# Kernel tuning notes

Hardware: AMD Instinct MI355X
Metric: run time of the kernel (lower is better)

Reference implementation:

```python
import jax, jax.numpy as jnp
import numpy as np

EPS = 1e-7
INF = 1e8
NUM_CLASSES = 80
SOFT_CENTER_RADIUS = 3.0
TOPK = 13
IOU_WEIGHT = 3.0
ALPHA = 1.0
BETA = 6.0
IMG = 640.0


def pairwise_iou(b1, b2):
    # b1: (B,N,4), b2: (B,M,4) in xyxy -> (B,N,M) IoU (mmdet BboxOverlaps2D, eps=1e-6)
    a1 = (b1[..., 2] - b1[..., 0]) * (b1[..., 3] - b1[..., 1])
    a2 = (b2[..., 2] - b2[..., 0]) * (b2[..., 3] - b2[..., 1])
    lt = jnp.maximum(b1[:, :, None, :2], b2[:, None, :, :2])
    rb = jnp.minimum(b1[:, :, None, 2:], b2[:, None, :, 2:])
    wh = jnp.clip(rb - lt, 0.0)
    inter = wh[..., 0] * wh[..., 1]
    union = a1[:, :, None] + a2[:, None, :] - inter
    return inter / jnp.maximum(union, 1e-6)


def _forward(pred_bboxes, pred_scores, priors, gt_labels, gt_bboxes, pad_bbox_flag):
    B, P, _ = pred_bboxes.shape
    G = gt_bboxes.shape[1]
    dt = pred_bboxes.dtype
    labels = gt_labels[..., 0]            # (B,G) int
    pad = pad_bbox_flag[..., 0]           # (B,G) float
    prior_xy = priors[:, :2]              # (P,2)
    strides = priors[:, 2]                # (P,)

    # ---- inside-gt test (find_inside_points, box_dim=4): (B,P,G) bool
    lt_ = prior_xy[None, :, None, :] - gt_bboxes[:, None, :, :2]
    rb_ = gt_bboxes[:, None, :, 2:] - prior_xy[None, :, None, :]
    is_in_gts = jnp.minimum(lt_.min(-1), rb_.min(-1)) > 0        # (B,P,G)
    is_in_gts_f = is_in_gts.astype(dt) * pad[:, None, :]         # masked by pad flag
    valid_mask = is_in_gts_f.sum(-1) > 0                          # (B,P)

    # ---- get_pos_mask (TaskAligned metric top-k) -> fg_mask_pre_prior
    overlaps = pairwise_iou(gt_bboxes, pred_bboxes)               # (B,G,P)
    scores_sig = jax.nn.sigmoid(pred_scores)                      # (B,P,C)
    scores_g = jnp.take_along_axis(scores_sig.transpose(0, 2, 1), labels[:, :, None], axis=1)  # (B,G,P)
    align = (scores_g ** ALPHA) * (overlaps ** BETA)              # (B,G,P)
    in_gts_gp = is_in_gts.transpose(0, 2, 1).astype(dt)           # (B,G,P)
    metrics = align * in_gts_gp
    _, topk_idxs = jax.lax.top_k(metrics, TOPK)                   # (B,G,TOPK)
    bb = jnp.arange(B)[:, None, None]
    gg = jnp.arange(G)[None, :, None]
    cnt = jnp.zeros((B, G, P), dt).at[bb, gg, topk_idxs].add(1.0)
    cnt = cnt * pad[:, :, None]
    is_in_topk = jnp.where(cnt > 1, 0.0, cnt)
    pos_mask = is_in_topk * in_gts_gp * pad[:, :, None]           # (B,G,P)
    # select_highest_overlaps: resolve priors matched to >1 gt via max IoU
    fg_pre = pos_mask.sum(1)                                      # (B,P)
    max_gt = overlaps.argmax(1)                                   # (B,P)
    is_max = (jnp.arange(G)[None, None, :] == max_gt[:, :, None]).astype(dt)  # (B,P,G)
    pos_mask = jnp.where((fg_pre > 1)[:, None, :], is_max.transpose(0, 2, 1), pos_mask)
    fg_mask_pre_prior = pos_mask.sum(1) > 0                       # (B,P) bool

    # ---- soft center prior
    gt_center = (gt_bboxes[..., :2] + gt_bboxes[..., 2:]) / 2.0   # (B,G,2)
    dist = jnp.sqrt(((prior_xy[None, :, None, :] - gt_center[:, None, :, :]) ** 2).sum(-1)) \
           / strides[None, :, None]                               # (B,P,G)
    dist = dist * valid_mask[..., None]
    soft_center_prior = jnp.power(10.0, dist - SOFT_CENTER_RADIUS)

    # ---- IoU cost
    pairwise_ious = pairwise_iou(pred_bboxes, gt_bboxes)          # (B,P,G)
    iou_cost = -jnp.log(pairwise_ious + EPS) * IOU_WEIGHT

    # ---- soft classification cost (QFL-style)
    logits = jnp.take_along_axis(pred_scores.transpose(0, 2, 1), labels[:, :, None], axis=1)
    logits = logits.transpose(0, 2, 1)                            # (B,P,G)
    scale = pairwise_ious - jax.nn.sigmoid(logits)
    bce = jnp.logaddexp(0.0, logits) - logits * pairwise_ious     # BCEWithLogits(logits, ious)
    cls_cost = bce * scale ** 2

    cost = cls_cost + iou_cost + soft_center_prior
    cost = jnp.where(valid_mask[..., None], cost, INF)            # (B,P,G)

    # ---- dynamic-k matching
    topk_ious, _ = jax.lax.top_k(pairwise_ious.transpose(0, 2, 1), TOPK)  # (B,G,TOPK)
    dynamic_ks = jnp.maximum(topk_ious.sum(-1).astype(jnp.int32), 1)      # (B,G)
    num_gts = pad.sum(-1).astype(jnp.int32)                                # (B,)
    sorted_idx = jnp.argsort(cost, axis=1)                                 # (B,P,G)
    ranks = jnp.arange(P)[None, :, None]
    gt_valid = jnp.arange(G)[None, :] < num_gts[:, None]                   # (B,G)
    sel = (ranks < dynamic_ks[:, None, :]) & gt_valid[:, None, :]          # (B,P,G), in sorted order
    bb2 = jnp.arange(B)[:, None, None]
    gg2 = jnp.arange(G)[None, None, :]
    matching = jnp.zeros((B, P, G), dt).at[bb2, sorted_idx, gg2].set(sel.astype(dt))
    multi = matching.sum(-1) > 1                                           # (B,P)
    argmin = cost.argmin(-1)                                               # (B,P)
    onehot_min = (jnp.arange(G)[None, None, :] == argmin[:, :, None]).astype(dt)
    matching = jnp.where(multi[..., None], onehot_min, matching)
    fg = matching.sum(-1) > 0                                              # (B,P)
    matched_ious = (matching * pairwise_ious).sum(-1)                      # (B,P)
    matched_gt_inds = matching.argmax(-1)                                  # (B,P)

    # ---- dense outputs (torch scatters into full-size tensors; same values here)
    assigned_labels = jnp.where(fg, jnp.take_along_axis(labels, matched_gt_inds, axis=1), NUM_CLASSES)
    assigned_labels_weights = jnp.ones((B, P), dt)
    assigned_bboxes = jnp.where(fg[..., None],
                                jnp.take_along_axis(gt_bboxes, matched_gt_inds[..., None].repeat(4, -1), axis=1),
                                0.0)
    assign_metrics = jnp.where(fg, matched_ious, 0.0)
    return assigned_labels, assigned_labels_weights, assigned_bboxes, assign_metrics, fg_mask_pre_prior


def setup_inputs() -> dict:
    key = jax.random.key(0)
    ks = jax.random.split(key, 6)
    B, G, C = 16, 100, 80
    # priors: anchor-free grid for 640x640, strides (8,16,32) -> P = 8400
    grids = []
    for s in (8, 16, 32):
        n = 640 // s
        xs = (np.arange(n, dtype=np.float32) + 0.5) * s
        yy, xx = np.meshgrid(xs, xs, indexing='ij')
        g = np.stack([xx.ravel(), yy.ravel(),
                      np.full(n * n, s, np.float32), np.full(n * n, s, np.float32)], -1)
        grids.append(g)
    priors = jnp.asarray(np.concatenate(grids, 0), jnp.float32)  # (8400, 4)
    P = priors.shape[0]

    def rand_boxes(k, shape):
        kc, kw = jax.random.split(k)
        cxy = jax.random.uniform(kc, shape + (2,), minval=0.0, maxval=IMG)
        wh = jax.random.uniform(kw, shape + (2,), minval=8.0, maxval=256.0)
        lt = jnp.clip(cxy - wh / 2, 0.0, IMG)
        rb = jnp.clip(cxy + wh / 2, 0.0, IMG)
        return jnp.concatenate([lt, rb], -1)

    pred_bboxes = rand_boxes(ks[0], (B, P))
    pred_scores = jax.random.normal(ks[1], (B, P, C), jnp.float32) * 2.0 - 2.0
    gt_bboxes = rand_boxes(ks[2], (B, G))
    gt_labels = jax.random.randint(ks[3], (B, G, 1), 0, C)
    n_valid = jax.random.randint(ks[4], (B,), 1, G + 1)
    pad_bbox_flag = (jnp.arange(G)[None, :] < n_valid[:, None]).astype(jnp.float32)[..., None]
    return {"pred_bboxes": pred_bboxes, "pred_scores": pred_scores, "priors": priors,
            "gt_labels": gt_labels, "gt_bboxes": gt_bboxes, "pad_bbox_flag": pad_bbox_flag}


def reference(pred_bboxes, pred_scores, priors, gt_labels, gt_bboxes, pad_bbox_flag):
    return _forward(pred_bboxes, pred_scores, priors, gt_labels, gt_bboxes, pad_bbox_flag)
```

## Files before the change

### kernel.cpp

```cpp
#include <hip/hip_runtime.h>
#include <cstdint>
#include <climits>
#include <cstddef>

#define TK 13
#define MAXG 128
#define CAP 192
#define NW 4
#define MCAP 24576
#define MAXCH 160

__device__ __forceinline__ float iou_fn(const float4 pb, const float4 gb){
  float pa = (pb.z - pb.x) * (pb.w - pb.y);
  float ga = (gb.z - gb.x) * (gb.w - gb.y);
  float ltx = fmaxf(pb.x, gb.x), lty = fmaxf(pb.y, gb.y);
  float rbx = fminf(pb.z, gb.z), rby = fminf(pb.w, gb.w);
  float w = fmaxf(rbx - ltx, 0.0f), h = fmaxf(rby - lty, 0.0f);
  float inter = w * h;
  float uni = pa + ga - inter;
  return inter / fmaxf(uni, 1e-6f);
}

__device__ __forceinline__ float sigmoid_f(float x){ return 1.0f / (1.0f + expf(-x)); }

__device__ __forceinline__ float cost_full(float iou, float s, float dist){
  float sig = sigmoid_f(s);
  float iouc = -logf(iou + 1e-7f) * 3.0f;
  float scale = iou - sig;
  float bce = fmaxf(s, 0.0f) + log1pf(expf(-fabsf(s))) - s * iou;
  float cls = bce * scale * scale;
  float soft = powf(10.0f, dist - 3.0f);
  return cls + iouc + soft;
}

__device__ __forceinline__ void bfly_max_u64(unsigned long long &v, int &l){
  #pragma unroll
  for (int off = 32; off >= 1; off >>= 1){
    unsigned long long ov = __shfl_xor(v, off);
    int ol = __shfl_xor(l, off);
    if (ov > v){ v = ov; l = ol; }
  }
}

__device__ __forceinline__ unsigned long long squeeze13(unsigned long long* buf, int& cnt, int lane){
  unsigned long long e0 = (lane < cnt) ? buf[lane] : 0ull;
  unsigned long long e1 = (lane + 64 < cnt) ? buf[lane + 64] : 0ull;
  unsigned long long e2 = (lane + 128 < cnt) ? buf[lane + 128] : 0ull;
  if (e0 < e2){ unsigned long long t = e0; e0 = e2; e2 = t; }
  if (e0 < e1){ unsigned long long t = e0; e0 = e1; e1 = t; }
  if (e1 < e2){ unsigned long long t = e1; e1 = e2; e2 = t; }
  unsigned long long T = 0;
  for (int r = 0; r < TK; ++r){
    unsigned long long m = e0; int l = lane;
    bfly_max_u64(m, l);
    if (lane == 0) buf[r] = m;
    T = m;
    if (lane == l){ e0 = e1; e1 = e2; e2 = 0ull; }
  }
  cnt = TK;
  return T;
}

__global__ __launch_bounds__(256) void k_valid(
    const float4* __restrict__ priors, const float4* __restrict__ pred_bboxes,
    const float4* __restrict__ gtb, const float* __restrict__ pad,
    unsigned long long* __restrict__ vmask, unsigned int* __restrict__ acc,
    unsigned int* __restrict__ mcnt,
    float4* __restrict__ predAB, float4* __restrict__ prAB, float* __restrict__ strC,
    int P, int G, int nCh)
{
  int b = blockIdx.y;
  int p = blockIdx.x * 256 + threadIdx.x;
  if (b == 0 && p == 0) *mcnt = 0u;
  __shared__ float4 sg[MAXG];
  __shared__ float sp[MAXG];
  for (int i = threadIdx.x; i < G; i += 256){ sg[i] = gtb[b*G + i]; sp[i] = pad[b*G + i]; }
  __syncthreads();
  int lane = threadIdx.x & 63;
  int ch = p >> 6;
  bool inb = p < P;
  float4 pr = inb ? priors[p] : make_float4(0,0,0,0);
  float4 pb = inb ? pred_bboxes[(size_t)b*P + p] : make_float4(0,0,0,0);
  bool v = false;
  if (inb){
    #pragma unroll 4
    for (int g = 0; g < G; ++g){
      float4 gb = sg[g];
      bool ig = (pr.x > gb.x) && (pr.y > gb.y) && (gb.z > pr.x) && (gb.w > pr.y);
      v = v || (ig && sp[g] > 0.5f);
    }
    acc[(size_t)b * P + p] = 0u;
  }
  unsigned long long m = __ballot(v);
  if (lane == 0 && ch < nCh) vmask[(size_t)b * nCh + ch] = m;
  float inf = __builtin_inff();
  float x1 = inb ? pb.x : inf,  y1 = inb ? pb.y : inf;
  float x2 = inb ? pb.z : -inf, y2 = inb ? pb.w : -inf;
  float px1 = inb ? pr.x : inf,  py1 = inb ? pr.y : inf;
  float px2 = inb ? pr.x : -inf, py2 = inb ? pr.y : -inf;
  #pragma unroll
  for (int off = 32; off >= 1; off >>= 1){
    x1 = fminf(x1, __shfl_xor(x1, off));  y1 = fminf(y1, __shfl_xor(y1, off));
    x2 = fmaxf(x2, __shfl_xor(x2, off));  y2 = fmaxf(y2, __shfl_xor(y2, off));
    px1 = fminf(px1, __shfl_xor(px1, off)); py1 = fminf(py1, __shfl_xor(py1, off));
    px2 = fmaxf(px2, __shfl_xor(px2, off)); py2 = fmaxf(py2, __shfl_xor(py2, off));
  }
  if (lane == 0 && ch < nCh){
    predAB[(size_t)b * nCh + ch] = make_float4(x1, y1, x2, y2);
    if (b == 0){ prAB[ch] = make_float4(px1, py1, px2, py2); strC[ch] = pr.z; }
  }
}

__global__ __launch_bounds__(256) void k_scan(
    const float4* __restrict__ pred_bboxes, const float* __restrict__ pred_scores,
    const float4* __restrict__ priors, const int* __restrict__ gt_labels,
    const float4* __restrict__ gtbb, const float* __restrict__ pad,
    const unsigned long long* __restrict__ vmask,
    const float4* __restrict__ predAB, const float4* __restrict__ prAB,
    const float* __restrict__ strC,
    unsigned int* __restrict__ acc, unsigned int* __restrict__ mcnt,
    unsigned int* __restrict__ mlist,
    int P, int G, int C, int nCh)
{
  int bg = blockIdx.x;
  if (pad[bg] <= 0.5f) return;
  int b = bg / G;
  int g = bg - b * G;
  int tid = threadIdx.x;
  int lane = tid & 63;
  int wv = tid >> 6;
  float4 gb = gtbb[bg];
  int lbl = gt_labels[bg];
  float gcx = (gb.x + gb.z) * 0.5f, gcy = (gb.y + gb.w) * 0.5f;
  size_t bP = (size_t)b * P;
  const unsigned long long* vmb = vmask + (size_t)b * nCh;
  const float4* pAB = predAB + (size_t)b * nCh;
  const unsigned B1E8 = __float_as_uint(1e8f);

  __shared__ unsigned long long bufM[NW*CAP], bufC[NW*CAP], bufI[NW*CAP];
  __shared__ uint2 sgeo[MAXCH];
  __shared__ unsigned long long svm[MAXCH];
  __shared__ unsigned int shwC, shwM, shwI;
  if (tid == 0){ shwC = 0xFFFFFFFFu; shwM = 0u; shwI = 0u; }
  for (int ch = tid; ch < nCh; ch += 256){
    float4 pA = pAB[ch];
    float4 rA = prAB[ch];
    float strc = strC[ch];
    bool geoI = !(pA.x < gb.z && pA.z > gb.x && pA.y < gb.w && pA.w > gb.y);
    bool geoM = !(rA.z > gb.x && rA.x < gb.z && rA.w > gb.y && rA.y < gb.w);
    float dxr = fmaxf(0.0f, fmaxf(rA.x - gcx, gcx - rA.z));
    float dyr = fmaxf(0.0f, fmaxf(rA.y - gcy, gcy - rA.w));
    float drr = sqrtf(dxr*dxr + dyr*dyr) / strc;
    sgeo[ch] = make_uint2((geoI ? 1u : 0u) | (geoM ? 2u : 0u), __float_as_uint(drr));
    svm[ch] = vmb[ch];
  }
  __syncthreads();
  unsigned long long* bM = bufM + wv*CAP;
  unsigned long long* bC = bufC + wv*CAP;
  unsigned long long* bI = bufI + wv*CAP;

  int cntM = 0, cntC = 0, cntI = 0;
  int zM = 0, zC = 0;
  unsigned long long Tm = 0ull, Tc = 0ull;
  unsigned long long Ti = 0x00000000FFFFFFFFull;
  unsigned cbits = 0xFFFFFFFFu, mBbits = 0u, iBb = 0u;
  float thr = 1e30f, mB = 0.0f;
  unsigned long long laneLT = (1ull << lane) - 1ull;

  for (int c = wv; c < nCh; c += NW){
    { unsigned sC = shwC; if (sC < cbits){ cbits = sC;
        thr = 3.0f + log10f(__uint_as_float(cbits) * 1.00002f + 1e-6f); } }
    { unsigned sM = shwM; if (sM > mBbits){ mBbits = sM; mB = __uint_as_float(sM); } }
    { unsigned sI = shwI; if (sI > iBb) iBb = sI; }
    uint2 ge = sgeo[c];
    bool geoI = (ge.x & 1u) != 0u;
    bool geoM = (ge.x & 2u) != 0u;
    float drr = __uint_as_float(ge.y);
    bool poolM = (zM >= TK) || (mBbits > 0u);
    bool poolC = (zC >= TK) || (cbits < B1E8);
    bool skipMt = geoM && poolM;
    bool skipCt = (drr > thr) && poolC;
    if (!(geoI && skipMt && skipCt)){
      int p = c * 64 + lane;
      bool inb = p < P;
      float4 pb = inb ? pred_bboxes[bP + p] : make_float4(0,0,0,0);
      float iou = iou_fn(pb, gb);
      unsigned long long keyI = ((unsigned long long)__float_as_uint(iou) << 32) | (unsigned)p;
      bool candI = inb && (keyI > Ti) && !((unsigned)(keyI >> 32) < iBb);
      if (cntI > CAP - 64){
        Ti = squeeze13(bI, cntI, lane);
        unsigned ib = (unsigned)(Ti >> 32);
        if (ib > iBb) iBb = ib;
        if (lane == 0 && ib) atomicMax(&shwI, ib);
        candI = candI && (keyI > Ti) && !((unsigned)(keyI >> 32) < iBb);
      }
      { unsigned long long mk = __ballot(candI);
        if (mk){ int off = cntI + __popcll(mk & laneLT); if (candI) bI[off] = keyI; cntI += __popcll(mk); } }
      if (!(skipMt && skipCt)){
        float4 pr = inb ? priors[p] : make_float4(0,0,0,0);
        bool vb = inb && (((svm[c] >> lane) & 1ull) != 0ull);
        bool ig = inb && (pr.x > gb.x) && (pr.y > gb.y) && (gb.z > pr.x) && (gb.w > pr.y);
        bool pos = ig && (iou > 0.0f);
        float i2 = iou * iou;
        float bnd = (i2 * i2) * i2 * 1.000002f;
        bool needm = pos && !(bnd < mB);
        float dist = 0.0f; bool needc = false;
        if (vb){
          float dx = pr.x - gcx, dy = pr.y - gcy;
          dist = sqrtf(dx*dx + dy*dy) / pr.z;
          needc = !(dist > thr);
        }
        float sc = 0.0f;
        if (needm || needc) sc = pred_scores[(bP + p) * C + lbl];
        unsigned long long keyM = 0;
        if (__ballot(needm)){
          float met = sigmoid_f(sc) * powf(iou, 6.0f);
          if (needm)
            keyM = ((unsigned long long)__float_as_uint(met) << 32)
                 | (unsigned)~(unsigned)((p << 1) | 1);
        }
        if (zM < TK && inb && !pos)
          keyM = (unsigned long long)(unsigned)~(unsigned)((p << 1) | (ig ? 1 : 0));
        bool candM = (keyM != 0ull) && (keyM > Tm) && !((unsigned)(keyM >> 32) < mBbits);
        unsigned long long keyC = 0;
        if (zC < TK && inb && !vb)
          keyC = ~(((unsigned long long)__float_as_uint(1e8f) << 32) | (unsigned)p);
        if (__ballot(needc)){
          float cst = cost_full(iou, sc, dist);
          if (needc)
            keyC = ~(((unsigned long long)__float_as_uint(cst) << 32) | (unsigned)p);
        }
        bool candC = (keyC != 0ull) && (keyC > Tc) && !((unsigned)((~keyC) >> 32) > cbits);
        if (cntM > CAP - 64){
          Tm = squeeze13(bM, cntM, lane);
          unsigned tb = (unsigned)(Tm >> 32);
          if (tb > mBbits){ mBbits = tb; mB = __uint_as_float(tb); }
          if (lane == 0 && tb) atomicMax(&shwM, tb);
          candM = candM && (keyM > Tm) && !((unsigned)(keyM >> 32) < mBbits);
        }
        { unsigned long long mk = __ballot(candM);
          if (mk){
            int off = cntM + __popcll(mk & laneLT);
            if (candM) bM[off] = keyM;
            cntM += __popcll(mk);
            unsigned long long zk = __ballot(candM && !pos);
            zM += __popcll(zk);
          } }
        if (cntC > CAP - 64){
          Tc = squeeze13(bC, cntC, lane);
          unsigned cb = (unsigned)((~Tc) >> 32);
          if (cb < cbits){ cbits = cb;
            thr = 3.0f + log10f(__uint_as_float(cbits) * 1.00002f + 1e-6f); }
          if (lane == 0) atomicMin(&shwC, cb);
          candC = candC && (keyC > Tc) && !((unsigned)((~keyC) >> 32) > cbits);
        }
        { unsigned long long mk = __ballot(candC);
          if (mk){
            int off = cntC + __popcll(mk & laneLT);
            if (candC) bC[off] = keyC;
            cntC += __popcll(mk);
            unsigned long long zk = __ballot(candC && !vb);
            zC += __popcll(zk);
          } }
      }
    }
  }

  squeeze13(bI, cntI, lane);
  squeeze13(bM, cntM, lane);
  squeeze13(bC, cntC, lane);
  __syncthreads();
  if (wv != 0) return;

  int w13 = lane / TK, r13 = lane - w13 * TK;
  int kd;
  {
    unsigned long long e = (lane < NW*TK) ? bufI[w13*CAP + r13] : 0ull;
    float ksum = 0.0f;
    for (int r = 0; r < TK; ++r){
      unsigned long long m = e; int l = lane;
      bfly_max_u64(m, l);
      ksum += __uint_as_float((unsigned)(m >> 32));
      if (lane == l) e = 0ull;
    }
    kd = (int)ksum; if (kd < 1) kd = 1;
  }
  {
    unsigned long long e = (lane < NW*TK) ? bufM[w13*CAP + r13] : 0ull;
    for (int r = 0; r < TK; ++r){
      unsigned long long m = e; int l = lane;
      bfly_max_u64(m, l);
      if (m == 0ull) break;
      if (lane == 0){
        unsigned ix = ~(unsigned)(m & 0xFFFFFFFFull);
        if (ix & 1u) atomicOr(&acc[bP + (ix >> 1)], 2u);
      }
      if (lane == l) e = 0ull;
    }
  }
  {
    unsigned long long e = (lane < NW*TK) ? bufC[w13*CAP + r13] : 0ull;
    for (int r = 0; r < kd; ++r){
      unsigned long long m = e; int l = lane;
      bfly_max_u64(m, l);
      if (m == 0ull) break;
      if (lane == 0){
        unsigned pp = (unsigned)((~m) & 0xFFFFFFFFull);
        unsigned old = atomicAdd(&acc[bP + pp], (1u << 17) | ((unsigned)g << 2));
        if ((old >> 17) == 1u){
          unsigned mi = atomicAdd(mcnt, 1u);
          if (mi < MCAP) mlist[mi] = (unsigned)(bP + pp);
        }
      }
      if (lane == l) e = 0ull;
    }
  }
}

__global__ __launch_bounds__(256) void k_final(
    const float4* __restrict__ pred_bboxes, const int* __restrict__ gt_labels,
    const float4* __restrict__ gtb, const unsigned int* __restrict__ acc,
    float* __restrict__ out, int B, int P, int G)
{
  int b = blockIdx.y;
  int p = blockIdx.x * 256 + threadIdx.x;
  __shared__ float4 sg[MAXG];
  __shared__ int sl[MAXG];
  for (int i = threadIdx.x; i < G; i += 256){
    sg[i] = gtb[b*G + i]; sl[i] = gt_labels[b*G + i];
  }
  __syncthreads();
  if (p >= P) return;
  size_t o = (size_t)b * P + p;
  unsigned int w = acc[o];
  int cnt = (int)(w >> 17);
  bool fg = cnt > 0;
  int mg = (cnt == 1) ? (int)((w >> 2) & 0x7FFFu) : 0;
  float4 pb = pred_bboxes[o];
  size_t BP = (size_t)B * P;
  out[o] = fg ? (float)sl[mg] : 80.0f;
  out[BP + o] = 1.0f;
  float4 ob = fg ? sg[mg] : make_float4(0.f, 0.f, 0.f, 0.f);
  ((float4*)(out + 2*BP))[o] = ob;
  out[6*BP + o] = fg ? iou_fn(pb, sg[mg]) : 0.0f;
  out[7*BP + o] = ((w >> 1) & 1u) ? 1.0f : 0.0f;
}

__global__ __launch_bounds__(256) void k_multi(
    const float4* __restrict__ pred_bboxes, const float* __restrict__ pred_scores,
    const float4* __restrict__ priors, const int* __restrict__ gt_labels,
    const float4* __restrict__ gtb, const unsigned long long* __restrict__ vmask,
    const unsigned int* __restrict__ mcnt, const unsigned int* __restrict__ mlist,
    float* __restrict__ out, int B, int P, int G, int C, int nCh)
{
  unsigned n = *mcnt; if (n > MCAP) n = MCAP;
  int lane = threadIdx.x & 63;
  int wid = (blockIdx.x * (blockDim.x >> 6)) + (threadIdx.x >> 6);
  int nw = gridDim.x * (blockDim.x >> 6);
  size_t BP = (size_t)B * P;
  for (unsigned i = wid; i < n; i += nw){
    unsigned o = mlist[i];
    int b = o / P;
    int p = o - b * P;
    float4 pb = pred_bboxes[o];
    bool vld = (vmask[(size_t)b * nCh + (p >> 6)] >> (p & 63)) & 1ull;
    int mg = 0;
    if (vld){
      float4 pr = priors[p];
      const float* srow = pred_scores + (size_t)o * C;
      unsigned long long best = 0xFFFFFFFFFFFFFFFFull;
      for (int g0 = lane; g0 < G; g0 += 64){
        float4 gbx = gtb[b*G + g0];
        float iou = iou_fn(pb, gbx);
        float s = srow[gt_labels[b*G + g0]];
        float gcx = (gbx.x + gbx.z) * 0.5f, gcy = (gbx.y + gbx.w) * 0.5f;
        float dx = pr.x - gcx, dy = pr.y - gcy;
        float dist = sqrtf(dx*dx + dy*dy) / pr.z;
        float cc = cost_full(iou, s, dist);
        unsigned long long k = ((unsigned long long)__float_as_uint(cc) << 32) | (unsigned)g0;
        if (k < best) best = k;
      }
      #pragma unroll
      for (int off = 32; off >= 1; off >>= 1){
        unsigned long long ov = __shfl_xor(best, off);
        if (ov < best) best = ov;
      }
      mg = (int)(best & 0xFFFFFFFFull);
    }
    if (lane == 0){
      float4 gbx = gtb[b*G + mg];
      out[o] = (float)gt_labels[b*G + mg];
      ((float4*)(out + 2*BP))[o] = gbx;
      out[6*BP + o] = iou_fn(pb, gbx);
    }
  }
}

extern "C" void kernel_launch(void* const* d_in, const int* in_sizes, int n_in,
                              void* d_out, int out_size, void* d_ws, size_t ws_size,
                              hipStream_t stream)
{
  const float4* pred_bboxes = (const float4*)d_in[0];
  const float*  pred_scores = (const float*)d_in[1];
  const float4* priors      = (const float4*)d_in[2];
  const int*    gt_labels   = (const int*)d_in[3];
  const float4* gt_bboxes   = (const float4*)d_in[4];
  const float*  pad         = (const float*)d_in[5];
  int P = in_sizes[2] / 4;
  int B = in_sizes[0] / (P * 4);
  int C = in_sizes[1] / (B * P);
  int G = in_sizes[4] / (B * 4);
  int BG = B * G;
  int nCh = (P + 63) >> 6;

  uint8_t* ws = (uint8_t*)d_ws;
  size_t off = 0;
  unsigned long long* vmask = (unsigned long long*)(ws + off); off += (size_t)B * nCh * 8;
  unsigned int* acc = (unsigned int*)(ws + off);               off += (size_t)B * P * 4;
  off = (off + 15) & ~(size_t)15;
  unsigned int* mcnt = (unsigned int*)(ws + off);              off += 16;
  unsigned int* mlist = (unsigned int*)(ws + off);             off += (size_t)MCAP * 4;
  off = (off + 15) & ~(size_t)15;
  float4* predAB = (float4*)(ws + off);                        off += (size_t)B * nCh * 16;
  float4* prAB = (float4*)(ws + off);                          off += (size_t)nCh * 16;
  float* strC = (float*)(ws + off);                            off += (size_t)nCh * 4;
  float* out = (float*)d_out;

  dim3 gridA((P + 255) / 256, B);
  k_valid<<<gridA, 256, 0, stream>>>(priors, pred_bboxes, gt_bboxes, pad,
                                     vmask, acc, mcnt, predAB, prAB, strC, P, G, nCh);
  k_scan<<<BG, NW*64, 0, stream>>>(pred_bboxes, pred_scores, priors, gt_labels,
                                   gt_bboxes, pad, vmask, predAB, prAB, strC,
                                   acc, mcnt, mlist, P, G, C, nCh);
  k_final<<<gridA, 256, 0, stream>>>(pred_bboxes, gt_labels, gt_bboxes, acc, out, B, P, G);
  k_multi<<<64, 256, 0, stream>>>(pred_bboxes, pred_scores, priors, gt_labels, gt_bboxes,
                                  vmask, mcnt, mlist, out, B, P, G, C, nCh);
}
```

Before: 273.5 us.

## Merge final and multi-match kernels into one launch; prefetch pred boxes in scan

The per-prior finalize kernel and the multi-match resolution kernel are combined into one launch. Extra blocks per batch handle the multi-match list, and finalize threads skip writing outputs for priors matched by several GTs, so the two kernels no longer write the same locations. The scan loop also software-prefetches the next chunk's predicted box so its load overlaps the current chunk's work. This removes one kernel launch and the serialization between the two tail kernels, at the cost of some extra register pressure in the scan loop.

```diff
diff --git a/kernel.cpp b/kernel.cpp
--- a/kernel.cpp
+++ b/kernel.cpp
@@ -9,6 +9,7 @@
 #define NW 4
 #define MCAP 24576
 #define MAXCH 160
+#define MBX 8
 
 __device__ __forceinline__ float iou_fn(const float4 pb, const float4 gb){
   float pa = (pb.z - pb.x) * (pb.w - pb.y);
@@ -167,7 +168,16 @@
   float thr = 1e30f, mB = 0.0f;
   unsigned long long laneLT = (1ull << lane) - 1ull;
 
-  for (int c = wv; c < nCh; c += NW){
+  int c0 = wv;
+  int pf = c0 * 64 + lane;
+  bool inb = (c0 < nCh) && (pf < P);
+  float4 pb = inb ? pred_bboxes[bP + pf] : make_float4(0,0,0,0);
+  for (int c = c0; c < nCh; c += NW){
+    int cn = c + NW;
+    int pn = cn * 64 + lane;
+    bool inbn = (cn < nCh) && (pn < P);
+    float4 pbn = make_float4(0,0,0,0);
+    if (inbn) pbn = pred_bboxes[bP + pn];
     { unsigned sC = shwC; if (sC < cbits){ cbits = sC;
         thr = 3.0f + log10f(__uint_as_float(cbits) * 1.00002f + 1e-6f); } }
     { unsigned sM = shwM; if (sM > mBbits){ mBbits = sM; mB = __uint_as_float(sM); } }
@@ -182,8 +192,6 @@
     bool skipCt = (drr > thr) && poolC;
     if (!(geoI && skipMt && skipCt)){
       int p = c * 64 + lane;
-      bool inb = p < P;
-      float4 pb = inb ? pred_bboxes[bP + p] : make_float4(0,0,0,0);
       float iou = iou_fn(pb, gb);
       unsigned long long keyI = ((unsigned long long)__float_as_uint(iou) << 32) | (unsigned)p;
       bool candI = inb && (keyI > Ti) && !((unsigned)(keyI >> 32) < iBb);
@@ -264,6 +272,7 @@
           } }
       }
     }
+    pb = pbn; inb = inbn;
   }
 
   squeeze13(bI, cntI, lane);
@@ -317,11 +326,59 @@
   }
 }
 
-__global__ __launch_bounds__(256) void k_final(
-    const float4* __restrict__ pred_bboxes, const int* __restrict__ gt_labels,
-    const float4* __restrict__ gtb, const unsigned int* __restrict__ acc,
-    float* __restrict__ out, int B, int P, int G)
+__global__ __launch_bounds__(256) void k_fm(
+    const float4* __restrict__ pred_bboxes, const float* __restrict__ pred_scores,
+    const float4* __restrict__ priors, const int* __restrict__ gt_labels,
+    const float4* __restrict__ gtb, const unsigned long long* __restrict__ vmask,
+    const unsigned int* __restrict__ acc,
+    const unsigned int* __restrict__ mcnt, const unsigned int* __restrict__ mlist,
+    float* __restrict__ out, int B, int P, int G, int C, int nCh, int nDecX)
 {
+  size_t BP = (size_t)B * P;
+  if ((int)blockIdx.x >= nDecX){
+    unsigned n = *mcnt; if (n > MCAP) n = MCAP;
+    int lane = threadIdx.x & 63;
+    int widx = ((int)blockIdx.y * MBX + ((int)blockIdx.x - nDecX)) * (blockDim.x >> 6)
+             + ((int)threadIdx.x >> 6);
+    int nw = gridDim.y * MBX * (blockDim.x >> 6);
+    for (unsigned i = widx; i < n; i += nw){
+      unsigned o = mlist[i];
+      int b = o / P;
+      int p = o - b * P;
+      float4 pb = pred_bboxes[o];
+      bool vld = (vmask[(size_t)b * nCh + (p >> 6)] >> (p & 63)) & 1ull;
+      int mg = 0;
+      if (vld){
+        float4 pr = priors[p];
+        const float* srow = pred_scores + (size_t)o * C;
+        unsigned long long best = 0xFFFFFFFFFFFFFFFFull;
+        for (int g0 = lane; g0 < G; g0 += 64){
+          float4 gbx = gtb[b*G + g0];
+          float iou = iou_fn(pb, gbx);
+          float s = srow[gt_labels[b*G + g0]];
+          float gcx = (gbx.x + gbx.z) * 0.5f, gcy = (gbx.y + gbx.w) * 0.5f;
+          float dx = pr.x - gcx, dy = pr.y - gcy;
+          float dist = sqrtf(dx*dx + dy*dy) / pr.z;
+          float cc = cost_full(iou, s, dist);
+          unsigned long long k = ((unsigned long long)__float_as_uint(cc) << 32) | (unsigned)g0;
+          if (k < best) best = k;
+        }
+        #pragma unroll
+        for (int off = 32; off >= 1; off >>= 1){
+          unsigned long long ov = __shfl_xor(best, off);
+          if (ov < best) best = ov;
+        }
+        mg = (int)(best & 0xFFFFFFFFull);
+      }
+      if (lane == 0){
+        float4 gbx = gtb[b*G + mg];
+        out[o] = (float)gt_labels[b*G + mg];
+        ((float4*)(out + 2*BP))[o] = gbx;
+        out[6*BP + o] = iou_fn(pb, gbx);
+      }
+    }
+    return;
+  }
   int b = blockIdx.y;
   int p = blockIdx.x * 256 + threadIdx.x;
   __shared__ float4 sg[MAXG];
@@ -334,66 +391,16 @@
   size_t o = (size_t)b * P + p;
   unsigned int w = acc[o];
   int cnt = (int)(w >> 17);
+  out[BP + o] = 1.0f;
+  out[7*BP + o] = ((w >> 1) & 1u) ? 1.0f : 0.0f;
+  if (cnt > 1) return;
   bool fg = cnt > 0;
-  int mg = (cnt == 1) ? (int)((w >> 2) & 0x7FFFu) : 0;
+  int mg = fg ? (int)((w >> 2) & 0x7FFFu) : 0;
   float4 pb = pred_bboxes[o];
-  size_t BP = (size_t)B * P;
   out[o] = fg ? (float)sl[mg] : 80.0f;
-  out[BP + o] = 1.0f;
   float4 ob = fg ? sg[mg] : make_float4(0.f, 0.f, 0.f, 0.f);
   ((float4*)(out + 2*BP))[o] = ob;
   out[6*BP + o] = fg ? iou_fn(pb, sg[mg]) : 0.0f;
-  out[7*BP + o] = ((w >> 1) & 1u) ? 1.0f : 0.0f;
-}
-
-__global__ __launch_bounds__(256) void k_multi(
-    const float4* __restrict__ pred_bboxes, const float* __restrict__ pred_scores,
-    const float4* __restrict__ priors, const int* __restrict__ gt_labels,
-    const float4* __restrict__ gtb, const unsigned long long* __restrict__ vmask,
-    const unsigned int* __restrict__ mcnt, const unsigned int* __restrict__ mlist,
-    float* __restrict__ out, int B, int P, int G, int C, int nCh)
-{
-  unsigned n = *mcnt; if (n > MCAP) n = MCAP;
-  int lane = threadIdx.x & 63;
-  int wid = (blockIdx.x * (blockDim.x >> 6)) + (threadIdx.x >> 6);
-  int nw = gridDim.x * (blockDim.x >> 6);
-  size_t BP = (size_t)B * P;
-  for (unsigned i = wid; i < n; i += nw){
-    unsigned o = mlist[i];
-    int b = o / P;
-    int p = o - b * P;
-    float4 pb = pred_bboxes[o];
-    bool vld = (vmask[(size_t)b * nCh + (p >> 6)] >> (p & 63)) & 1ull;
-    int mg = 0;
-    if (vld){
-      float4 pr = priors[p];
-      const float* srow = pred_scores + (size_t)o * C;
-      unsigned long long best = 0xFFFFFFFFFFFFFFFFull;
-      for (int g0 = lane; g0 < G; g0 += 64){
-        float4 gbx = gtb[b*G + g0];
-        float iou = iou_fn(pb, gbx);
-        float s = srow[gt_labels[b*G + g0]];
-        float gcx = (gbx.x + gbx.z) * 0.5f, gcy = (gbx.y + gbx.w) * 0.5f;
-        float dx = pr.x - gcx, dy = pr.y - gcy;
-        float dist = sqrtf(dx*dx + dy*dy) / pr.z;
-        float cc = cost_full(iou, s, dist);
-        unsigned long long k = ((unsigned long long)__float_as_uint(cc) << 32) | (unsigned)g0;
-        if (k < best) best = k;
-      }
-      #pragma unroll
-      for (int off = 32; off >= 1; off >>= 1){
-        unsigned long long ov = __shfl_xor(best, off);
-        if (ov < best) best = ov;
-      }
-      mg = (int)(best & 0xFFFFFFFFull);
-    }
-    if (lane == 0){
-      float4 gbx = gtb[b*G + mg];
-      out[o] = (float)gt_labels[b*G + mg];
-      ((float4*)(out + 2*BP))[o] = gbx;
-      out[6*BP + o] = iou_fn(pb, gbx);
-    }
-  }
 }
 
 extern "C" void kernel_launch(void* const* d_in, const int* in_sizes, int n_in,
@@ -426,13 +433,15 @@
   float* strC = (float*)(ws + off);                            off += (size_t)nCh * 4;
   float* out = (float*)d_out;
 
-  dim3 gridA((P + 255) / 256, B);
+  int nDecX = (P + 255) / 256;
+  dim3 gridA(nDecX, B);
+  dim3 gridF(nDecX + MBX, B);
   k_valid<<<gridA, 256, 0, stream>>>(priors, pred_bboxes, gt_bboxes, pad,
                                      vmask, acc, mcnt, predAB, prAB, strC, P, G, nCh);
   k_scan<<<BG, NW*64, 0, stream>>>(pred_bboxes, pred_scores, priors, gt_labels,
                                    gt_bboxes, pad, vmask, predAB, prAB, strC,
                                    acc, mcnt, mlist, P, G, C, nCh);
-  k_final<<<gridA, 256, 0, stream>>>(pred_bboxes, gt_labels, gt_bboxes, acc, out, B, P, G);
-  k_multi<<<64, 256, 0, stream>>>(pred_bboxes, pred_scores, priors, gt_labels, gt_bboxes,
-                                  vmask, mcnt, mlist, out, B, P, G, C, nCh);
-}
+  k_fm<<<gridF, 256, 0, stream>>>(pred_bboxes, pred_scores, priors, gt_labels,
+                                  gt_bboxes, vmask, acc, mcnt, mlist, out,
+                                  B, P, G, C, nCh, nDecX);
+}
```

Result: faster. 262.6 us (-4.0%).
